# Kernel tuning notes

Measured on AMD Instinct MI355X. Metric: run time of the kernel, lower is better.

Reference implementation:

```python
import jax, jax.numpy as jnp
import numpy as np

K = 512            # initial_num_embeddings (all active)
D = 64             # embedding_dim
COMMITMENT_COST = 0.25


def setup_inputs() -> dict:
    key = jax.random.key(0)
    k1, k2 = jax.random.split(key)
    inputs = jax.random.normal(k1, (64, 2048, D), dtype=jnp.float32)
    # nn.Embedding initialized uniform(-1/K, 1/K)
    embedding = jax.random.uniform(k2, (K, D), dtype=jnp.float32,
                                   minval=-1.0 / K, maxval=1.0 / K)
    return {"inputs": inputs, "embedding": embedding}


def reference(inputs, embedding):
    input_shape = inputs.shape
    flat = inputs.reshape(-1, embedding.shape[1])          # [N, D]

    # All codes active at init, so active_indices == arange(K) (identity).
    distances = (jnp.sum(flat * flat, axis=1, keepdims=True)
                 + jnp.sum(embedding * embedding, axis=1)
                 - 2.0 * (flat @ embedding.T))
    encoding_indices = jnp.argmin(distances, axis=1)       # [N]

    # One-hot scatter encoding, then quantize via matmul (as in original)
    encodings = jax.nn.one_hot(encoding_indices, K, dtype=flat.dtype)  # [N, K]
    quantized = (encodings @ embedding).reshape(input_shape)

    e_latent_loss = jnp.mean((jax.lax.stop_gradient(quantized) - inputs) ** 2)
    q_latent_loss = jnp.mean((quantized - jax.lax.stop_gradient(inputs)) ** 2)
    vq_loss = q_latent_loss + COMMITMENT_COST * e_latent_loss

    # Straight-through estimator
    quantized_st = inputs + jax.lax.stop_gradient(quantized - inputs)

    avg_probs = jnp.mean(encodings, axis=0)                # [K]
    perplexity = jnp.exp(-jnp.sum(avg_probs * jnp.log(avg_probs + 1e-10)))

    return vq_loss, quantized_st, perplexity, encodings, encoding_indices
```

## Files before the change

### kernel.cpp

```cpp
#include <hip/hip_runtime.h>
#include <math.h>

#define N_ROWS 131072
#define DIM 64
#define KCODES 512

#define O_LOSS 0
#define O_Q    1ull
#define O_PERP 8388609ull
#define O_ENC  8388610ull
#define O_IDX  75497474ull

#define AMB_WIN 1.5e-4f
#define AMB_CAP 32768

using sh8   = __attribute__((ext_vector_type(8))) short;
using f32x4 = __attribute__((ext_vector_type(4))) float;

__device__ __forceinline__ unsigned bf16rne_bits(float x) {
    unsigned u = __float_as_uint(x);
    return u + 0x7fffu + ((u >> 16) & 1u);
}
__device__ __forceinline__ void bf16split(float v, unsigned short& h, unsigned short& s) {
    unsigned hb = bf16rne_bits(v);
    float hf = __uint_as_float(hb & 0xffff0000u);
    unsigned lb = bf16rne_bits(v - hf);
    h = (unsigned short)(hb >> 16);
    s = (unsigned short)(lb >> 16);
}

__global__ void vq_prep(const float* __restrict__ emb, float* __restrict__ bsq,
                        int* __restrict__ counts, double* __restrict__ loss_acc,
                        int* __restrict__ amb_count,
                        unsigned short* __restrict__ Bhi, unsigned short* __restrict__ Blo) {
#pragma clang fp contract(off)
    int t = blockIdx.x * 256 + threadIdx.x;
    if (t < KCODES * DIM) {
        int c = t >> 6, d = t & 63;
        unsigned short h, s;
        bf16split(emb[t], h, s);
        int CT = c >> 4, col = c & 15, hh = d >> 5, j = d & 7, lh = (d >> 3) & 3;
        int addr = ((CT * 2 + hh) * 64 + (lh * 16 + col)) * 8 + j;
        Bhi[addr] = h;
        Blo[addr] = s;
    }
    if (t < KCODES) {
        const float* e = emb + (size_t)t * DIM;
        float r[8];
#pragma unroll
        for (int j = 0; j < 8; ++j) { float v = e[j]; r[j] = v * v; }
#pragma unroll
        for (int i = 8; i < 64; i += 8)
#pragma unroll
            for (int j = 0; j < 8; ++j) { float v = e[i + j]; r[j] = r[j] + v * v; }
        bsq[t] = ((r[0] + r[1]) + (r[2] + r[3])) + ((r[4] + r[5]) + (r[6] + r[7]));
        counts[t] = 0;
    }
    if (t == 0) { *loss_acc = 0.0; *amb_count = 0; }
}

__global__ __launch_bounds__(256) void vq_mfma(
    const float* __restrict__ x, const float* __restrict__ emb,
    const float* __restrict__ bsq,
    const unsigned short* __restrict__ Bhi, const unsigned short* __restrict__ Blo,
    int* __restrict__ counts, double* __restrict__ loss_acc, float* __restrict__ out,
    int* __restrict__ amb_count, int* __restrict__ amb_rows)
{
    __shared__ int    idx_l[64];
    __shared__ double wsum[4];

    const int tid  = threadIdx.x;
    const int l    = tid & 63;
    const int w    = tid >> 6;
    const int row0 = blockIdx.x * 64;
    const int arow = row0 + w * 16 + (l & 15);
    const int kb   = (l >> 4) * 8;

    float4 a0 = *reinterpret_cast<const float4*>(&x[(size_t)arow * 64 + kb]);
    float4 a1 = *reinterpret_cast<const float4*>(&x[(size_t)arow * 64 + kb + 4]);
    float4 a2 = *reinterpret_cast<const float4*>(&x[(size_t)arow * 64 + kb + 32]);
    float4 a3 = *reinterpret_cast<const float4*>(&x[(size_t)arow * 64 + kb + 36]);
    unsigned short ah[16], al[16];
    {
        float av[16] = {a0.x,a0.y,a0.z,a0.w, a1.x,a1.y,a1.z,a1.w,
                        a2.x,a2.y,a2.z,a2.w, a3.x,a3.y,a3.z,a3.w};
#pragma unroll
        for (int i = 0; i < 16; ++i) bf16split(av[i], ah[i], al[i]);
    }
    sh8 ah0 = *reinterpret_cast<sh8*>(&ah[0]), ah1 = *reinterpret_cast<sh8*>(&ah[8]);
    sh8 al0 = *reinterpret_cast<sh8*>(&al[0]), al1 = *reinterpret_cast<sh8*>(&al[8]);

    float m1[4], m2[4];
    int   i1[4];
#pragma unroll
    for (int j = 0; j < 4; ++j) { m1[j] = 3.4e38f; m2[j] = 3.4e38f; i1[j] = 0; }

    const int col = l & 15;
#pragma unroll 4
    for (int CT = 0; CT < 32; ++CT) {
        sh8 bh0 = *reinterpret_cast<const sh8*>(&Bhi[(size_t)(CT * 2 + 0) * 512 + l * 8]);
        sh8 bh1 = *reinterpret_cast<const sh8*>(&Bhi[(size_t)(CT * 2 + 1) * 512 + l * 8]);
        sh8 bl0 = *reinterpret_cast<const sh8*>(&Blo[(size_t)(CT * 2 + 0) * 512 + l * 8]);
        sh8 bl1 = *reinterpret_cast<const sh8*>(&Blo[(size_t)(CT * 2 + 1) * 512 + l * 8]);
        f32x4 acc = {0.f, 0.f, 0.f, 0.f};
        acc = __builtin_amdgcn_mfma_f32_16x16x32_bf16(ah0, bh0, acc, 0, 0, 0);
        acc = __builtin_amdgcn_mfma_f32_16x16x32_bf16(ah1, bh1, acc, 0, 0, 0);
        acc = __builtin_amdgcn_mfma_f32_16x16x32_bf16(ah0, bl0, acc, 0, 0, 0);
        acc = __builtin_amdgcn_mfma_f32_16x16x32_bf16(ah1, bl1, acc, 0, 0, 0);
        acc = __builtin_amdgcn_mfma_f32_16x16x32_bf16(al0, bh0, acc, 0, 0, 0);
        acc = __builtin_amdgcn_mfma_f32_16x16x32_bf16(al1, bh1, acc, 0, 0, 0);

        int code = CT * 16 + col;
        float bs = bsq[code];
#pragma unroll
        for (int j = 0; j < 4; ++j) {
            float tt = bs - 2.0f * acc[j];
            if (tt < m1[j]) { m2[j] = m1[j]; m1[j] = tt; i1[j] = code; }
            else if (tt < m2[j]) { m2[j] = tt; }
        }
    }

#pragma unroll
    for (int off = 8; off >= 1; off >>= 1)
#pragma unroll
        for (int j = 0; j < 4; ++j) {
            float ov1 = __shfl_xor(m1[j], off, 64);
            int   oi1 = __shfl_xor(i1[j], off, 64);
            float ov2 = __shfl_xor(m2[j], off, 64);
            float hi  = fmaxf(m1[j], ov1);
            m2[j] = fminf(fminf(m2[j], ov2), hi);
            if (ov1 < m1[j] || (ov1 == m1[j] && oi1 < i1[j])) { m1[j] = ov1; i1[j] = oi1; }
        }

    if ((l & 15) == 0) {
#pragma unroll
        for (int j = 0; j < 4; ++j) {
            int r_loc = w * 16 + ((l >> 4) << 2) + j;
            idx_l[r_loc] = i1[j];
            out[O_IDX + row0 + r_loc] = (float)i1[j];
            atomicAdd(&counts[i1[j]], 1);
            if (m2[j] - m1[j] <= AMB_WIN) {
                int slot = atomicAdd(amb_count, 1);
                if (slot < AMB_CAP) amb_rows[slot] = row0 + r_loc;
            }
        }
    }
    __syncthreads();

    double lsum = 0.0;
#pragma unroll 4
    for (int k = 0; k < 16; ++k) {
        int i = tid + k * 256;
        int r = i >> 6, d = i & 63;
        int id = idx_l[r];
        float xv = x[(size_t)(row0 + r) * 64 + d];
        float ev = emb[(size_t)id * 64 + d];
        float diff = ev - xv;
        out[O_Q + (size_t)(row0 + r) * 64 + d] = xv + diff;
        lsum += (double)diff * (double)diff;
    }

    float2* enc2 = reinterpret_cast<float2*>(out + O_ENC + (size_t)row0 * KCODES);
#pragma unroll 4
    for (int k = 0; k < 64; ++k) {
        int i = tid + k * 256;
        int r = i >> 8;
        int c = (i & 255) * 2;
        int id = idx_l[r];
        float2 v;
        v.x = (c     == id) ? 1.f : 0.f;
        v.y = (c + 1 == id) ? 1.f : 0.f;
        enc2[i] = v;
    }

#pragma unroll
    for (int off = 32; off >= 1; off >>= 1) lsum += __shfl_xor(lsum, off, 64);
    if ((tid & 63) == 0) wsum[tid >> 6] = lsum;
    __syncthreads();
    if (tid == 0) atomicAdd(loss_acc, wsum[0] + wsum[1] + wsum[2] + wsum[3]);
}

__global__ __launch_bounds__(256, 2) void vq_fixup(
    const float* __restrict__ x, const float* __restrict__ emb,
    const float* __restrict__ bsq, int* __restrict__ counts,
    double* __restrict__ loss_acc, float* __restrict__ out,
    const int* __restrict__ amb_count, const int* __restrict__ amb_rows)
{
#pragma clang fp contract(off)
    __shared__ float Xt[64 * 34];
    __shared__ float Et[64 * 68];
    __shared__ float sx_l[32];
    __shared__ int   rowid_l[32];

    const int tid = threadIdx.x;
    const int tx  = tid & 15;
    const int ty  = tid >> 4;
    int n = *amb_count; if (n > AMB_CAP) n = AMB_CAP;

    for (int base = blockIdx.x * 32; base < n; base += gridDim.x * 32) {
        const int nrows = min(32, n - base);
        if (tid < 32) {
            int e = base + tid;
            rowid_l[tid] = amb_rows[e < n ? e : (n - 1)];
        }
        __syncthreads();

#pragma unroll
        for (int k = 0; k < 8; ++k) {
            int i = tid + k * 256;
            int r = i >> 6, d = i & 63;
            Xt[d * 34 + r] = x[(size_t)rowid_l[r] * 64 + d];
        }
        __syncthreads();

        if (tid < 32) {
            float rr[8];
#pragma unroll
            for (int j = 0; j < 8; ++j) { float v = Xt[j * 34 + tid]; rr[j] = v * v; }
#pragma unroll
            for (int i = 8; i < 64; i += 8)
#pragma unroll
                for (int j = 0; j < 8; ++j) { float v = Xt[(i + j) * 34 + tid]; rr[j] = rr[j] + v * v; }
            sx_l[tid] = ((rr[0] + rr[1]) + (rr[2] + rr[3])) + ((rr[4] + rr[5]) + (rr[6] + rr[7]));
        }
        __syncthreads();

        float b1[2]; int bi[2];
#pragma unroll
        for (int m = 0; m < 2; ++m) { b1[m] = 3.4e38f; bi[m] = 0; }

        for (int ch = 0; ch < 8; ++ch) {
            if (ch > 0) __syncthreads();
#pragma unroll
            for (int k = 0; k < 4; ++k) {
                int i = tid + k * 256;
                int c = i >> 4, c4 = i & 15;
                float4 v = *reinterpret_cast<const float4*>(&emb[(size_t)(ch * 64 + c) * 64 + c4 * 4]);
                Et[(c4 * 4 + 0) * 68 + c] = v.x;
                Et[(c4 * 4 + 1) * 68 + c] = v.y;
                Et[(c4 * 4 + 2) * 68 + c] = v.z;
                Et[(c4 * 4 + 3) * 68 + c] = v.w;
            }
            __syncthreads();

            float acc[2][4];
#pragma unroll
            for (int m = 0; m < 2; ++m)
#pragma unroll
                for (int nn = 0; nn < 4; ++nn) acc[m][nn] = 0.f;

#pragma unroll 8
            for (int d = 0; d < 64; ++d) {
                float2 a = *reinterpret_cast<const float2*>(&Xt[d * 34 + ty * 2]);
                float4 b = *reinterpret_cast<const float4*>(&Et[d * 68 + tx * 4]);
                float av[2] = {a.x, a.y};
                float bv[4] = {b.x, b.y, b.z, b.w};
#pragma unroll
                for (int m = 0; m < 2; ++m)
#pragma unroll
                    for (int nn = 0; nn < 4; ++nn)
                        acc[m][nn] = fmaf(av[m], bv[nn], acc[m][nn]);
            }

            const int cbase = ch * 64 + tx * 4;
            float4 bs4 = *reinterpret_cast<const float4*>(&bsq[cbase]);
            float bs[4] = {bs4.x, bs4.y, bs4.z, bs4.w};
#pragma unroll
            for (int m = 0; m < 2; ++m) {
                float sxm = sx_l[ty * 2 + m];
#pragma unroll
                for (int nn = 0; nn < 4; ++nn) {
                    float S  = sxm + bs[nn];
                    float dd = S - 2.0f * acc[m][nn];
                    if (dd < b1[m]) { b1[m] = dd; bi[m] = cbase + nn; }
                }
            }
        }

#pragma unroll
        for (int off = 8; off >= 1; off >>= 1)
#pragma unroll
            for (int m = 0; m < 2; ++m) {
                float ov = __shfl_xor(b1[m], off, 64);
                int   oi = __shfl_xor(bi[m], off, 64);
                if (ov < b1[m] || (ov == b1[m] && oi < bi[m])) { b1[m] = ov; bi[m] = oi; }
            }

        if (tx == 0) {
#pragma unroll
            for (int m = 0; m < 2; ++m) {
                int rl = ty * 2 + m;
                if (rl < nrows) {
                    int row = rowid_l[rl];
                    int fi  = bi[m];
                    int old = (int)out[O_IDX + row];
                    if (fi != old) {
                        out[O_IDX + row] = (float)fi;
                        out[O_ENC + (size_t)row * KCODES + old] = 0.f;
                        out[O_ENC + (size_t)row * KCODES + fi]  = 1.f;
                        atomicAdd(&counts[old], -1);
                        atomicAdd(&counts[fi], 1);
                        double dl = 0.0;
                        for (int d = 0; d < 64; ++d) {
                            float xv   = Xt[d * 34 + rl];
                            float dn   = emb[(size_t)fi * 64 + d] - xv;
                            float dold = emb[(size_t)old * 64 + d] - xv;
                            out[O_Q + (size_t)row * 64 + d] = xv + dn;
                            dl += (double)dn * (double)dn - (double)dold * (double)dold;
                        }
                        atomicAdd(loss_acc, dl);
                    }
                }
            }
        }
        __syncthreads();
    }
}

__global__ void vq_fin(const int* __restrict__ counts, const double* __restrict__ loss_acc,
                       float* __restrict__ out) {
    int t = threadIdx.x;
    double h = 0.0;
    for (int c = t; c < KCODES; c += 256) {
        double p = (double)counts[c] / (double)N_ROWS;
        h += p * log(p + 1e-10);
    }
#pragma unroll
    for (int off = 32; off >= 1; off >>= 1) h += __shfl_xor(h, off, 64);
    __shared__ double ws[4];
    if ((t & 63) == 0) ws[t >> 6] = h;
    __syncthreads();
    if (t == 0) {
        double H = ws[0] + ws[1] + ws[2] + ws[3];
        out[O_PERP] = (float)exp(-H);
        out[O_LOSS] = (float)(1.25 * (*loss_acc) / (double)(N_ROWS * DIM));
    }
}

extern "C" void kernel_launch(void* const* d_in, const int* in_sizes, int n_in,
                              void* d_out, int out_size, void* d_ws, size_t ws_size,
                              hipStream_t stream) {
    const float* x   = (const float*)d_in[0];
    const float* emb = (const float*)d_in[1];
    float* out = (float*)d_out;

    float*          bsq       = (float*)d_ws;
    int*            counts    = (int*)((char*)d_ws + 2048);
    double*         loss_acc  = (double*)((char*)d_ws + 4096);
    int*            amb_count = (int*)((char*)d_ws + 4112);
    int*            amb_rows  = (int*)((char*)d_ws + 4160);
    unsigned short* Bhi       = (unsigned short*)((char*)d_ws + 139264);
    unsigned short* Blo       = (unsigned short*)((char*)d_ws + 212992);

    vq_prep<<<128, 256, 0, stream>>>(emb, bsq, counts, loss_acc, amb_count, Bhi, Blo);
    vq_mfma<<<N_ROWS / 64, 256, 0, stream>>>(x, emb, bsq, Bhi, Blo, counts, loss_acc, out,
                                             amb_count, amb_rows);
    vq_fixup<<<1024, 256, 0, stream>>>(x, emb, bsq, counts, loss_acc, out,
                                       amb_count, amb_rows);
    vq_fin<<<1, 256, 0, stream>>>(counts, loss_acc, out);
}
```

Measured before the change: 192.9 us.

## Zero one-hot output in a separate pass and process two row tiles per block

A new vq_zero kernel clears the whole encodings buffer with wide float4 grid-stride stores, and also resets the counters that vq_prep used to reset. The main MFMA kernel then writes only the single 1.0 per row, instead of writing every element of the one-hot row itself. Each block now handles 128 rows as two 16-row tiles per wave, so each loaded embedding fragment feeds twice as many MFMAs. In exchange the dense write becomes a separate launch followed by scattered single-float stores, and register pressure rises. The fixup path must also clear the old 1.0 for any row whose index it changes.

```diff
diff --git a/kernel.cpp b/kernel.cpp
--- a/kernel.cpp
+++ b/kernel.cpp
@@ -10,6 +10,9 @@
 #define O_PERP 8388609ull
 #define O_ENC  8388610ull
 #define O_IDX  75497474ull
+
+#define ENC_F4_BASE 8388612ull
+#define ENC_F4_CNT  16777215ull
 
 #define AMB_WIN 1.5e-4f
 #define AMB_CAP 32768
@@ -29,9 +32,22 @@
     s = (unsigned short)(lb >> 16);
 }
 
+__global__ __launch_bounds__(256) void vq_zero(float* __restrict__ out, int* __restrict__ counts,
+                                               double* __restrict__ loss_acc, int* __restrict__ amb_count) {
+    size_t tid = (size_t)blockIdx.x * 256 + threadIdx.x;
+    float4 z = make_float4(0.f, 0.f, 0.f, 0.f);
+    float4* base = reinterpret_cast<float4*>(out + ENC_F4_BASE);
+    size_t stride = (size_t)gridDim.x * 256;
+    for (size_t i = tid; i < ENC_F4_CNT; i += stride) base[i] = z;
+    if (tid < KCODES) counts[tid] = 0;
+    if (tid == 0) {
+        out[O_ENC] = 0.f; out[O_ENC + 1] = 0.f;
+        out[O_ENC + 67108862ull] = 0.f; out[O_ENC + 67108863ull] = 0.f;
+        *loss_acc = 0.0; *amb_count = 0;
+    }
+}
+
 __global__ void vq_prep(const float* __restrict__ emb, float* __restrict__ bsq,
-                        int* __restrict__ counts, double* __restrict__ loss_acc,
-                        int* __restrict__ amb_count,
                         unsigned short* __restrict__ Bhi, unsigned short* __restrict__ Blo) {
 #pragma clang fp contract(off)
     int t = blockIdx.x * 256 + threadIdx.x;
@@ -54,9 +70,7 @@
 #pragma unroll
             for (int j = 0; j < 8; ++j) { float v = e[i + j]; r[j] = r[j] + v * v; }
         bsq[t] = ((r[0] + r[1]) + (r[2] + r[3])) + ((r[4] + r[5]) + (r[6] + r[7]));
-        counts[t] = 0;
-    }
-    if (t == 0) { *loss_acc = 0.0; *amb_count = 0; }
+    }
 }
 
 __global__ __launch_bounds__(256) void vq_mfma(
@@ -66,90 +80,106 @@
     int* __restrict__ counts, double* __restrict__ loss_acc, float* __restrict__ out,
     int* __restrict__ amb_count, int* __restrict__ amb_rows)
 {
-    __shared__ int    idx_l[64];
+    __shared__ int    idx_l[128];
     __shared__ double wsum[4];
 
     const int tid  = threadIdx.x;
     const int l    = tid & 63;
     const int w    = tid >> 6;
-    const int row0 = blockIdx.x * 64;
-    const int arow = row0 + w * 16 + (l & 15);
+    const int row0 = blockIdx.x * 128;
     const int kb   = (l >> 4) * 8;
-
-    float4 a0 = *reinterpret_cast<const float4*>(&x[(size_t)arow * 64 + kb]);
-    float4 a1 = *reinterpret_cast<const float4*>(&x[(size_t)arow * 64 + kb + 4]);
-    float4 a2 = *reinterpret_cast<const float4*>(&x[(size_t)arow * 64 + kb + 32]);
-    float4 a3 = *reinterpret_cast<const float4*>(&x[(size_t)arow * 64 + kb + 36]);
-    unsigned short ah[16], al[16];
-    {
+    const int rA   = row0 + w * 16 + (l & 15);
+    const int rB   = rA + 64;
+
+    sh8 ahf[2][2], alf[2][2];
+#pragma unroll
+    for (int t = 0; t < 2; ++t) {
+        const float* xr = &x[(size_t)(t == 0 ? rA : rB) * 64 + kb];
+        float4 a0 = *reinterpret_cast<const float4*>(xr);
+        float4 a1 = *reinterpret_cast<const float4*>(xr + 4);
+        float4 a2 = *reinterpret_cast<const float4*>(xr + 32);
+        float4 a3 = *reinterpret_cast<const float4*>(xr + 36);
         float av[16] = {a0.x,a0.y,a0.z,a0.w, a1.x,a1.y,a1.z,a1.w,
                         a2.x,a2.y,a2.z,a2.w, a3.x,a3.y,a3.z,a3.w};
+        unsigned short ah[16], al[16];
 #pragma unroll
         for (int i = 0; i < 16; ++i) bf16split(av[i], ah[i], al[i]);
-    }
-    sh8 ah0 = *reinterpret_cast<sh8*>(&ah[0]), ah1 = *reinterpret_cast<sh8*>(&ah[8]);
-    sh8 al0 = *reinterpret_cast<sh8*>(&al[0]), al1 = *reinterpret_cast<sh8*>(&al[8]);
-
-    float m1[4], m2[4];
-    int   i1[4];
-#pragma unroll
-    for (int j = 0; j < 4; ++j) { m1[j] = 3.4e38f; m2[j] = 3.4e38f; i1[j] = 0; }
+        ahf[t][0] = *reinterpret_cast<sh8*>(&ah[0]);
+        ahf[t][1] = *reinterpret_cast<sh8*>(&ah[8]);
+        alf[t][0] = *reinterpret_cast<sh8*>(&al[0]);
+        alf[t][1] = *reinterpret_cast<sh8*>(&al[8]);
+    }
+
+    float m1[2][4], m2[2][4];
+    int   i1[2][4];
+#pragma unroll
+    for (int t = 0; t < 2; ++t)
+#pragma unroll
+        for (int j = 0; j < 4; ++j) { m1[t][j] = 3.4e38f; m2[t][j] = 3.4e38f; i1[t][j] = 0; }
 
     const int col = l & 15;
-#pragma unroll 4
+#pragma unroll 2
     for (int CT = 0; CT < 32; ++CT) {
         sh8 bh0 = *reinterpret_cast<const sh8*>(&Bhi[(size_t)(CT * 2 + 0) * 512 + l * 8]);
         sh8 bh1 = *reinterpret_cast<const sh8*>(&Bhi[(size_t)(CT * 2 + 1) * 512 + l * 8]);
         sh8 bl0 = *reinterpret_cast<const sh8*>(&Blo[(size_t)(CT * 2 + 0) * 512 + l * 8]);
         sh8 bl1 = *reinterpret_cast<const sh8*>(&Blo[(size_t)(CT * 2 + 1) * 512 + l * 8]);
-        f32x4 acc = {0.f, 0.f, 0.f, 0.f};
-        acc = __builtin_amdgcn_mfma_f32_16x16x32_bf16(ah0, bh0, acc, 0, 0, 0);
-        acc = __builtin_amdgcn_mfma_f32_16x16x32_bf16(ah1, bh1, acc, 0, 0, 0);
-        acc = __builtin_amdgcn_mfma_f32_16x16x32_bf16(ah0, bl0, acc, 0, 0, 0);
-        acc = __builtin_amdgcn_mfma_f32_16x16x32_bf16(ah1, bl1, acc, 0, 0, 0);
-        acc = __builtin_amdgcn_mfma_f32_16x16x32_bf16(al0, bh0, acc, 0, 0, 0);
-        acc = __builtin_amdgcn_mfma_f32_16x16x32_bf16(al1, bh1, acc, 0, 0, 0);
-
         int code = CT * 16 + col;
         float bs = bsq[code];
 #pragma unroll
-        for (int j = 0; j < 4; ++j) {
-            float tt = bs - 2.0f * acc[j];
-            if (tt < m1[j]) { m2[j] = m1[j]; m1[j] = tt; i1[j] = code; }
-            else if (tt < m2[j]) { m2[j] = tt; }
+        for (int t = 0; t < 2; ++t) {
+            f32x4 acc = {0.f, 0.f, 0.f, 0.f};
+            acc = __builtin_amdgcn_mfma_f32_16x16x32_bf16(ahf[t][0], bh0, acc, 0, 0, 0);
+            acc = __builtin_amdgcn_mfma_f32_16x16x32_bf16(ahf[t][1], bh1, acc, 0, 0, 0);
+            acc = __builtin_amdgcn_mfma_f32_16x16x32_bf16(ahf[t][0], bl0, acc, 0, 0, 0);
+            acc = __builtin_amdgcn_mfma_f32_16x16x32_bf16(ahf[t][1], bl1, acc, 0, 0, 0);
+            acc = __builtin_amdgcn_mfma_f32_16x16x32_bf16(alf[t][0], bh0, acc, 0, 0, 0);
+            acc = __builtin_amdgcn_mfma_f32_16x16x32_bf16(alf[t][1], bh1, acc, 0, 0, 0);
+#pragma unroll
+            for (int j = 0; j < 4; ++j) {
+                float tt = bs - 2.0f * acc[j];
+                if (tt < m1[t][j]) { m2[t][j] = m1[t][j]; m1[t][j] = tt; i1[t][j] = code; }
+                else if (tt < m2[t][j]) { m2[t][j] = tt; }
+            }
         }
     }
 
 #pragma unroll
     for (int off = 8; off >= 1; off >>= 1)
 #pragma unroll
-        for (int j = 0; j < 4; ++j) {
-            float ov1 = __shfl_xor(m1[j], off, 64);
-            int   oi1 = __shfl_xor(i1[j], off, 64);
-            float ov2 = __shfl_xor(m2[j], off, 64);
-            float hi  = fmaxf(m1[j], ov1);
-            m2[j] = fminf(fminf(m2[j], ov2), hi);
-            if (ov1 < m1[j] || (ov1 == m1[j] && oi1 < i1[j])) { m1[j] = ov1; i1[j] = oi1; }
-        }
+        for (int t = 0; t < 2; ++t)
+#pragma unroll
+            for (int j = 0; j < 4; ++j) {
+                float ov1 = __shfl_xor(m1[t][j], off, 64);
+                int   oi1 = __shfl_xor(i1[t][j], off, 64);
+                float ov2 = __shfl_xor(m2[t][j], off, 64);
+                float hi  = fmaxf(m1[t][j], ov1);
+                m2[t][j] = fminf(fminf(m2[t][j], ov2), hi);
+                if (ov1 < m1[t][j] || (ov1 == m1[t][j] && oi1 < i1[t][j])) { m1[t][j] = ov1; i1[t][j] = oi1; }
+            }
 
     if ((l & 15) == 0) {
 #pragma unroll
-        for (int j = 0; j < 4; ++j) {
-            int r_loc = w * 16 + ((l >> 4) << 2) + j;
-            idx_l[r_loc] = i1[j];
-            out[O_IDX + row0 + r_loc] = (float)i1[j];
-            atomicAdd(&counts[i1[j]], 1);
-            if (m2[j] - m1[j] <= AMB_WIN) {
-                int slot = atomicAdd(amb_count, 1);
-                if (slot < AMB_CAP) amb_rows[slot] = row0 + r_loc;
-            }
-        }
+        for (int t = 0; t < 2; ++t)
+#pragma unroll
+            for (int j = 0; j < 4; ++j) {
+                int r_loc = t * 64 + w * 16 + ((l >> 4) << 2) + j;
+                int id = i1[t][j];
+                idx_l[r_loc] = id;
+                out[O_IDX + row0 + r_loc] = (float)id;
+                out[O_ENC + (size_t)(row0 + r_loc) * KCODES + id] = 1.0f;
+                atomicAdd(&counts[id], 1);
+                if (m2[t][j] - m1[t][j] <= AMB_WIN) {
+                    int slot = atomicAdd(amb_count, 1);
+                    if (slot < AMB_CAP) amb_rows[slot] = row0 + r_loc;
+                }
+            }
     }
     __syncthreads();
 
     double lsum = 0.0;
 #pragma unroll 4
-    for (int k = 0; k < 16; ++k) {
+    for (int k = 0; k < 32; ++k) {
         int i = tid + k * 256;
         int r = i >> 6, d = i & 63;
         int id = idx_l[r];
@@ -158,19 +188,6 @@
         float diff = ev - xv;
         out[O_Q + (size_t)(row0 + r) * 64 + d] = xv + diff;
         lsum += (double)diff * (double)diff;
-    }
-
-    float2* enc2 = reinterpret_cast<float2*>(out + O_ENC + (size_t)row0 * KCODES);
-#pragma unroll 4
-    for (int k = 0; k < 64; ++k) {
-        int i = tid + k * 256;
-        int r = i >> 8;
-        int c = (i & 255) * 2;
-        int id = idx_l[r];
-        float2 v;
-        v.x = (c     == id) ? 1.f : 0.f;
-        v.y = (c + 1 == id) ? 1.f : 0.f;
-        enc2[i] = v;
     }
 
 #pragma unroll
@@ -352,9 +369,10 @@
     unsigned short* Bhi       = (unsigned short*)((char*)d_ws + 139264);
     unsigned short* Blo       = (unsigned short*)((char*)d_ws + 212992);
 
-    vq_prep<<<128, 256, 0, stream>>>(emb, bsq, counts, loss_acc, amb_count, Bhi, Blo);
-    vq_mfma<<<N_ROWS / 64, 256, 0, stream>>>(x, emb, bsq, Bhi, Blo, counts, loss_acc, out,
-                                             amb_count, amb_rows);
+    vq_zero<<<2048, 256, 0, stream>>>(out, counts, loss_acc, amb_count);
+    vq_prep<<<128, 256, 0, stream>>>(emb, bsq, Bhi, Blo);
+    vq_mfma<<<N_ROWS / 128, 256, 0, stream>>>(x, emb, bsq, Bhi, Blo, counts, loss_acc, out,
+                                              amb_count, amb_rows);
     vq_fixup<<<1024, 256, 0, stream>>>(x, emb, bsq, counts, loss_acc, out,
                                        amb_count, amb_rows);
     vq_fin<<<1, 256, 0, stream>>>(counts, loss_acc, out);
```

Measured after the change: 242.6 us. 1.26x slower.
